# Optimization experiments

Hardware: AMD Instinct MI355X
Metric: run time of the kernel (lower is better)

The kernel has to match this reference:

```python
import jax, jax.numpy as jnp
import numpy as np

I, H, W, S = 1024, 1024, 128, 64


def setup_inputs() -> dict:
    key = jax.random.key(0)
    ks = jax.random.split(key, 20)
    s = 1.0 / np.sqrt(H)  # torch LSTM/Linear init scale
    d = {
        "inputs": jax.random.normal(ks[0], (S, W, I), jnp.float32),
        "h1": jax.random.normal(ks[1], (H,), jnp.float32),
        "c1": jax.random.normal(ks[2], (H,), jnp.float32),
        "h2": jax.random.normal(ks[3], (H,), jnp.float32),
        "c2": jax.random.normal(ks[4], (H,), jnp.float32),
        "Wih1": jax.random.normal(ks[5], (4 * H, I), jnp.float32) * s,
        "Whh1": jax.random.normal(ks[6], (4 * H, H), jnp.float32) * s,
        "bih1": jax.random.normal(ks[7], (4 * H,), jnp.float32) * s,
        "bhh1": jax.random.normal(ks[8], (4 * H,), jnp.float32) * s,
        "Wih2": jax.random.normal(ks[9], (4 * H, H), jnp.float32) * s,
        "Whh2": jax.random.normal(ks[10], (4 * H, H), jnp.float32) * s,
        "bih2": jax.random.normal(ks[11], (4 * H,), jnp.float32) * s,
        "bhh2": jax.random.normal(ks[12], (4 * H,), jnp.float32) * s,
        "att_words": jax.random.normal(ks[13], (W,), jnp.float32),
        "att_sents": jax.random.normal(ks[14], (S,), jnp.float32),
        "Wf": jax.random.normal(ks[15], (1, H), jnp.float32) * s,
        "bf": jax.random.normal(ks[16], (1,), jnp.float32) * s,
    }
    return d


def _lstm_cell(x, h, c, Wih, Whh, bih, bhh):
    # torch gate order: i, f, g, o
    g = x @ Wih.T + h @ Whh.T + bih + bhh  # (4H,)
    i, f, gg, o = jnp.split(g, 4)
    c2 = jax.nn.sigmoid(f) * c + jax.nn.sigmoid(i) * jnp.tanh(gg)
    h2 = jax.nn.sigmoid(o) * jnp.tanh(c2)
    return h2, c2


def reference(inputs, h1, c1, h2, c2, Wih1, Whh1, bih1, bhh1,
              Wih2, Whh2, bih2, bhh2, att_words, att_sents, Wf, bf):
    aw = jax.nn.softmax(att_words)   # (W,)
    asn = jax.nn.softmax(att_sents)  # (S,)

    def word_step(carry, x):
        h, c = carry
        h, c = _lstm_cell(x, h, c, Wih1, Whh1, bih1, bhh1)
        return (h, c), h

    def sent_step(carry, sent):  # sent: (W, I)
        carry, hs = jax.lax.scan(word_step, carry, sent)  # hs: (W, H)
        enc = aw @ hs  # attention pooling over words -> (H,)
        # original detaches hidden state between sentences (forward identity)
        carry = (jax.lax.stop_gradient(carry[0]), jax.lax.stop_gradient(carry[1]))
        return carry, enc

    _, encs = jax.lax.scan(sent_step, (h1, c1), inputs)  # (S, H)

    def sent_lstm_step(carry, x):
        h, c = carry
        h, c = _lstm_cell(x, h, c, Wih2, Whh2, bih2, bhh2)
        return (h, c), h

    _, hs2 = jax.lax.scan(sent_lstm_step, (h2, c2), encs)  # (S, H)
    row = asn @ hs2  # (H,)
    out = jax.nn.sigmoid(row @ Wf.T + bf)  # (1,)
    return out.reshape(1, 1)
```

## Files before the change

### kernel.cpp

```cpp
#include <hip/hip_runtime.h>
#include <hip/hip_bf16.h>

#define NWG 256
#define NTH 256
#define T1  8192
#define SS  64
#define WW  128

typedef unsigned long long u64;
typedef unsigned int u32x4 __attribute__((ext_vector_type(4)));


__device__ __forceinline__ u64 aload(const u64* p) {
  return __hip_atomic_load(p, __ATOMIC_RELAXED, __HIP_MEMORY_SCOPE_AGENT);
}
__device__ __forceinline__ void aswap(u64* p, u64 v) {
  (void)__hip_atomic_exchange(p, v, __ATOMIC_RELAXED, __HIP_MEMORY_SCOPE_AGENT);
}
__device__ __forceinline__ u64 pack(float v, unsigned tag) {
  return ((u64)tag << 32) | (u64)__float_as_uint(v);
}
__device__ __forceinline__ float ftanh(float x) {
  return 1.f - 2.f / (1.f + __expf(2.f * x));
}

__device__ __forceinline__ void load32_sc1(const u64* p, u32x4& a, u32x4& b) {
  asm volatile("global_load_dwordx4 %0, %2, off sc1\n\t"
               "global_load_dwordx4 %1, %2, off offset:16 sc1\n\t"
               "s_waitcnt vmcnt(0)"
               : "=&v"(a), "=&v"(b) : "v"(p) : "memory");
}

#define SPIN4(BASE, TAG, DST) do {                                        \
    const u64* _q = (BASE) + ((size_t)tid << 2);                          \
    const unsigned _t = (unsigned)(TAG); u32x4 _a, _b;                    \
    for (;;) { load32_sc1(_q, _a, _b);                                    \
      if (__builtin_expect(_a.y == _t && _a.w == _t &&                    \
                           _b.y == _t && _b.w == _t, 1)) break; }         \
    float* _d = (DST) + (tid << 2);                                       \
    _d[0] = __uint_as_float(_a.x); _d[1] = __uint_as_float(_a.z);         \
    _d[2] = __uint_as_float(_b.x); _d[3] = __uint_as_float(_b.z);         \
  } while (0)

__global__ __launch_bounds__(NTH) __attribute__((amdgpu_waves_per_eu(1, 1)))
void lstm_hier_attn(const float* __restrict__ xin,
                    const float* __restrict__ h1_0, const float* __restrict__ c1_0,
                    const float* __restrict__ h2_0, const float* __restrict__ c2_0,
                    const float* __restrict__ Wih1, const float* __restrict__ Whh1,
                    const float* __restrict__ bih1, const float* __restrict__ bhh1,
                    const float* __restrict__ Wih2, const float* __restrict__ Whh2,
                    const float* __restrict__ bih2, const float* __restrict__ bhh2,
                    const float* __restrict__ attw, const float* __restrict__ atts,
                    const float* __restrict__ Wf,   const float* __restrict__ bfb,
                    u64* hbuf64, u64* encs64, u64* part64, float* out)
{
  const int wid = blockIdx.x;
  const int tid = threadIdx.x;
  const int wv  = tid >> 6;
  const int l   = tid & 63;
  const int u0  = wid << 2;

  __shared__ float wih_lds[16 * 1024];
  __shared__ float h_lds[2][1024];
  __shared__ float e_lds[2][1024];
  __shared__ float aw_lds[WW];
  __shared__ float as_lds[SS];
  __shared__ float fin_lds[4];

  if (tid == 0) {
    float m = -1e30f;
    for (int i = 0; i < WW; ++i) m = fmaxf(m, attw[i]);
    float ssum = 0.f;
    for (int i = 0; i < WW; ++i) { float e = __expf(attw[i] - m); aw_lds[i] = e; ssum += e; }
    float inv = 1.f / ssum;
    for (int i = 0; i < WW; ++i) aw_lds[i] *= inv;
    m = -1e30f;
    for (int i = 0; i < SS; ++i) m = fmaxf(m, atts[i]);
    ssum = 0.f;
    for (int i = 0; i < SS; ++i) { float e = __expf(atts[i] - m); as_lds[i] = e; ssum += e; }
    inv = 1.f / ssum;
    for (int i = 0; i < SS; ++i) as_lds[i] *= inv;
  }

  for (int q = 0; q < 64; ++q) {
    const int idx = (q << 8) + tid;
    const int rr = idx >> 10, col = idx & 1023;
    wih_lds[idx] = Wih1[(size_t)(((rr >> 2) << 10) + u0 + (rr & 3)) * 1024 + col];
  }
  float whh[4][16], bias[4];
#pragma unroll
  for (int g = 0; g < 4; ++g) {
    const int grow = (g << 10) + u0 + wv;
    bias[g] = bih1[grow] + bhh1[grow];
    const float* ph = Whh1 + (size_t)grow * 1024 + l;
#pragma unroll
    for (int m = 0; m < 16; ++m) whh[g][m] = ph[m << 6];
  }
#pragma unroll
  for (int g = 0; g < 4; ++g)
#pragma unroll
    for (int m = 0; m < 16; ++m) asm volatile("" : "+v"(whh[g][m]));

  float c   = c1_0[u0 + wv];
  float enc = 0.f, row = 0.f;
  const int rb0 = (0 + wv) << 10, rb1 = (4 + wv) << 10,
            rb2 = (8 + wv) << 10, rb3 = (12 + wv) << 10;
  __syncthreads();

  for (int k = 0; k < T1; ++k) {
    const int p = k & 1;
    const float* xrow = xin + (size_t)k * 1024;
    float a0 = 0.f, a1 = 0.f, a2 = 0.f, a3 = 0.f;
#pragma unroll
    for (int m = 0; m < 16; ++m) {
      const int cix = (m << 6) + l;
      const float x = xrow[cix];
      a0 += wih_lds[rb0 + cix] * x; a1 += wih_lds[rb1 + cix] * x;
      a2 += wih_lds[rb2 + cix] * x; a3 += wih_lds[rb3 + cix] * x;
    }

    if (k > 0) { SPIN4(hbuf64 + ((size_t)p << 10), k, h_lds[p]); }
    else {
      const float* s = h1_0 + (tid << 2); float* d = h_lds[0] + (tid << 2);
      d[0] = s[0]; d[1] = s[1]; d[2] = s[2]; d[3] = s[3];
    }
    __syncthreads();

#pragma unroll
    for (int m = 0; m < 16; ++m) {
      const float hv = h_lds[p][(m << 6) + l];
      a0 += whh[0][m] * hv; a1 += whh[1][m] * hv;
      a2 += whh[2][m] * hv; a3 += whh[3][m] * hv;
    }
#pragma unroll
    for (int mm = 1; mm < 64; mm <<= 1) {
      a0 += __shfl_xor(a0, mm); a1 += __shfl_xor(a1, mm);
      a2 += __shfl_xor(a2, mm); a3 += __shfl_xor(a3, mm);
    }
    const float ig = a0 + bias[0], fg = a1 + bias[1];
    const float gg = a2 + bias[2], og = a3 + bias[3];
    const float si = 1.f / (1.f + __expf(-ig));
    const float sf = 1.f / (1.f + __expf(-fg));
    const float so = 1.f / (1.f + __expf(-og));
    c = sf * c + si * ftanh(gg);
    const float h = so * ftanh(c);
    if (l == 0)
      aswap(&hbuf64[((size_t)((k + 1) & 1) << 10) + u0 + wv],
            pack(h, (unsigned)(k + 1)));
    const int wd = k & (WW - 1);
    const float e_new = enc + aw_lds[wd] * h;
    if (wd == WW - 1) {
      if (l == 0)
        aswap(&encs64[((size_t)(k >> 7) << 10) + u0 + wv],
              pack(e_new, (unsigned)((k >> 7) + 1)));
      enc = 0.f;
    } else enc = e_new;
  }

  __syncthreads();
  for (int q = 0; q < 64; ++q) {
    const int idx = (q << 8) + tid;
    const int rr = idx >> 10, col = idx & 1023;
    wih_lds[idx] = Wih2[(size_t)(((rr >> 2) << 10) + u0 + (rr & 3)) * 1024 + col];
  }
#pragma unroll
  for (int g = 0; g < 4; ++g) {
    const int grow = (g << 10) + u0 + wv;
    bias[g] = bih2[grow] + bhh2[grow];
    const float* ph = Whh2 + (size_t)grow * 1024 + l;
#pragma unroll
    for (int m = 0; m < 16; ++m) whh[g][m] = ph[m << 6];
  }
#pragma unroll
  for (int g = 0; g < 4; ++g)
#pragma unroll
    for (int m = 0; m < 16; ++m) asm volatile("" : "+v"(whh[g][m]));
  c = c2_0[u0 + wv];

  for (int s2 = 0; s2 < SS; ++s2) {
    const unsigned kg = (unsigned)(T1 + s2);
    const int p = (int)(kg & 1), pe = s2 & 1;
    SPIN4(encs64 + ((size_t)s2 << 10), (unsigned)(s2 + 1), e_lds[pe]);
    SPIN4(hbuf64 + ((size_t)p << 10), kg, h_lds[p]);
    if (s2 == 0) {
      const float* s = h2_0 + (tid << 2); float* d = h_lds[0] + (tid << 2);
      d[0] = s[0]; d[1] = s[1]; d[2] = s[2]; d[3] = s[3];
    }
    __syncthreads();

    float a0 = 0.f, a1 = 0.f, a2 = 0.f, a3 = 0.f;
#pragma unroll
    for (int m = 0; m < 16; ++m) {
      const int cix = (m << 6) + l;
      const float ev = e_lds[pe][cix];
      a0 += wih_lds[rb0 + cix] * ev; a1 += wih_lds[rb1 + cix] * ev;
      a2 += wih_lds[rb2 + cix] * ev; a3 += wih_lds[rb3 + cix] * ev;
      const float hv = h_lds[p][cix];
      a0 += whh[0][m] * hv; a1 += whh[1][m] * hv;
      a2 += whh[2][m] * hv; a3 += whh[3][m] * hv;
    }
#pragma unroll
    for (int mm = 1; mm < 64; mm <<= 1) {
      a0 += __shfl_xor(a0, mm); a1 += __shfl_xor(a1, mm);
      a2 += __shfl_xor(a2, mm); a3 += __shfl_xor(a3, mm);
    }
    const float ig = a0 + bias[0], fg = a1 + bias[1];
    const float gg = a2 + bias[2], og = a3 + bias[3];
    const float si = 1.f / (1.f + __expf(-ig));
    const float sf = 1.f / (1.f + __expf(-fg));
    const float so = 1.f / (1.f + __expf(-og));
    c = sf * c + si * ftanh(gg);
    const float h = so * ftanh(c);
    if (l == 0)
      aswap(&hbuf64[((size_t)((kg + 1) & 1) << 10) + u0 + wv], pack(h, kg + 1u));
    row += as_lds[s2] * h;
  }

  if (l == 0) fin_lds[wv] = row * Wf[u0 + wv];
  __syncthreads();
  if (tid == 0)
    aswap(&part64[wid],
          pack(fin_lds[0] + fin_lds[1] + fin_lds[2] + fin_lds[3], 1u));
  if (wid == 0) {
    u64 a;
    for (;;) { a = aload(&part64[tid]); if ((unsigned)(a >> 32) == 1u) break; }
    e_lds[0][tid] = __uint_as_float((unsigned)a);
    __syncthreads();
    if (wv == 0) {
      float pp = e_lds[0][l] + e_lds[0][64 + l] + e_lds[0][128 + l] + e_lds[0][192 + l];
#pragma unroll
      for (int mm = 1; mm < 64; mm <<= 1) pp += __shfl_xor(pp, mm);
      if (l == 0) out[0] = 1.f / (1.f + __expf(-(pp + bfb[0])));
    }
  }
}

extern "C" void kernel_launch(void* const* d_in, const int* in_sizes, int n_in,
                              void* d_out, int out_size, void* d_ws, size_t ws_size,
                              hipStream_t stream) {
  (void)in_sizes; (void)n_in; (void)out_size; (void)ws_size;
  const float* xin  = (const float*)d_in[0];
  const float* h1   = (const float*)d_in[1];
  const float* c1   = (const float*)d_in[2];
  const float* h2   = (const float*)d_in[3];
  const float* c2   = (const float*)d_in[4];
  const float* Wih1 = (const float*)d_in[5];
  const float* Whh1 = (const float*)d_in[6];
  const float* bih1 = (const float*)d_in[7];
  const float* bhh1 = (const float*)d_in[8];
  const float* Wih2 = (const float*)d_in[9];
  const float* Whh2 = (const float*)d_in[10];
  const float* bih2 = (const float*)d_in[11];
  const float* bhh2 = (const float*)d_in[12];
  const float* attw = (const float*)d_in[13];
  const float* atts = (const float*)d_in[14];
  const float* Wf   = (const float*)d_in[15];
  const float* bfb  = (const float*)d_in[16];

  u64* hbuf64 = (u64*)d_ws;
  u64* encs64 = hbuf64 + 2048;
  u64* part64 = encs64 + 65536;
  float* out  = (float*)d_out;

  hipMemsetAsync(d_ws, 0, (2048 + 65536 + 256) * sizeof(u64), stream);
  lstm_hier_attn<<<dim3(NWG), dim3(NTH), 0, stream>>>(
      xin, h1, c1, h2, c2, Wih1, Whh1, bih1, bhh1,
      Wih2, Whh2, bih2, bhh2, attw, atts, Wf, bfb,
      hbuf64, encs64, part64, out);
}
```

Baseline: 16.65 ms.

## Halve workgroup count and exchange hidden state as packed fp16 pairs

Regroups the persistent kernel from 256 workgroups of 4 waves into 128 workgroups of 8 waves, so each workgroup owns 8 hidden units and holds twice as many Wih rows in LDS. Each workgroup gathers its 8 new h values in LDS and publishes them as four tagged fp16-pair words. Readers then poll half as many 16-byte slots per step. The goal is to shrink the grid-wide spin-exchange payload and the number of participants in the per-step handoff. The cost is an extra __syncthreads per step, two waves per SIMD competing for compute, and fp16 rounding of the recurrent hidden state.

```diff
diff --git a/kernel.cpp b/kernel.cpp
--- a/kernel.cpp
+++ b/kernel.cpp
@@ -1,8 +1,8 @@
 #include <hip/hip_runtime.h>
-#include <hip/hip_bf16.h>
-
-#define NWG 256
-#define NTH 256
+#include <hip/hip_fp16.h>
+
+#define NWG 128
+#define NTH 512
 #define T1  8192
 #define SS  64
 #define WW  128
@@ -17,32 +17,29 @@
 __device__ __forceinline__ void aswap(u64* p, u64 v) {
   (void)__hip_atomic_exchange(p, v, __ATOMIC_RELAXED, __HIP_MEMORY_SCOPE_AGENT);
 }
-__device__ __forceinline__ u64 pack(float v, unsigned tag) {
+__device__ __forceinline__ u64 packf(float v, unsigned tag) {
   return ((u64)tag << 32) | (u64)__float_as_uint(v);
+}
+__device__ __forceinline__ unsigned pk2(float a, float b) {
+  __half2 h = __floats2half2_rn(a, b);
+  return *(unsigned*)&h;
+}
+__device__ __forceinline__ float2 upk2(unsigned u) {
+  __half2 h = *(__half2*)&u;
+  return __half22float2(h);
 }
 __device__ __forceinline__ float ftanh(float x) {
   return 1.f - 2.f / (1.f + __expf(2.f * x));
 }
 
-__device__ __forceinline__ void load32_sc1(const u64* p, u32x4& a, u32x4& b) {
-  asm volatile("global_load_dwordx4 %0, %2, off sc1\n\t"
-               "global_load_dwordx4 %1, %2, off offset:16 sc1\n\t"
-               "s_waitcnt vmcnt(0)"
-               : "=&v"(a), "=&v"(b) : "v"(p) : "memory");
-}
-
-#define SPIN4(BASE, TAG, DST) do {                                        \
-    const u64* _q = (BASE) + ((size_t)tid << 2);                          \
-    const unsigned _t = (unsigned)(TAG); u32x4 _a, _b;                    \
-    for (;;) { load32_sc1(_q, _a, _b);                                    \
-      if (__builtin_expect(_a.y == _t && _a.w == _t &&                    \
-                           _b.y == _t && _b.w == _t, 1)) break; }         \
-    float* _d = (DST) + (tid << 2);                                       \
-    _d[0] = __uint_as_float(_a.x); _d[1] = __uint_as_float(_a.z);         \
-    _d[2] = __uint_as_float(_b.x); _d[3] = __uint_as_float(_b.z);         \
-  } while (0)
-
-__global__ __launch_bounds__(NTH) __attribute__((amdgpu_waves_per_eu(1, 1)))
+__device__ __forceinline__ u32x4 load16_sc1(const void* p) {
+  u32x4 r;
+  asm volatile("global_load_dwordx4 %0, %1, off sc1\n\ts_waitcnt vmcnt(0)"
+               : "=&v"(r) : "v"(p) : "memory");
+  return r;
+}
+
+__global__ __launch_bounds__(NTH) __attribute__((amdgpu_waves_per_eu(2, 2)))
 void lstm_hier_attn(const float* __restrict__ xin,
                     const float* __restrict__ h1_0, const float* __restrict__ c1_0,
                     const float* __restrict__ h2_0, const float* __restrict__ c2_0,
@@ -58,14 +55,15 @@
   const int tid = threadIdx.x;
   const int wv  = tid >> 6;
   const int l   = tid & 63;
-  const int u0  = wid << 2;
-
-  __shared__ float wih_lds[16 * 1024];
+  const int u0  = wid << 3;
+
+  __shared__ float wih_lds[32 * 1024];
   __shared__ float h_lds[2][1024];
   __shared__ float e_lds[2][1024];
   __shared__ float aw_lds[WW];
   __shared__ float as_lds[SS];
-  __shared__ float fin_lds[4];
+  __shared__ float h_out[8];
+  __shared__ float fin_lds[8];
 
   if (tid == 0) {
     float m = -1e30f;
@@ -83,9 +81,9 @@
   }
 
   for (int q = 0; q < 64; ++q) {
-    const int idx = (q << 8) + tid;
+    const int idx = (q << 9) + tid;
     const int rr = idx >> 10, col = idx & 1023;
-    wih_lds[idx] = Wih1[(size_t)(((rr >> 2) << 10) + u0 + (rr & 3)) * 1024 + col];
+    wih_lds[idx] = Wih1[(size_t)(((rr >> 3) << 10) + u0 + (rr & 7)) * 1024 + col];
   }
   float whh[4][16], bias[4];
 #pragma unroll
@@ -103,8 +101,8 @@
 
   float c   = c1_0[u0 + wv];
   float enc = 0.f, row = 0.f;
-  const int rb0 = (0 + wv) << 10, rb1 = (4 + wv) << 10,
-            rb2 = (8 + wv) << 10, rb3 = (12 + wv) << 10;
+  const int rb0 = (0 * 8 + wv) << 10, rb1 = (1 * 8 + wv) << 10,
+            rb2 = (2 * 8 + wv) << 10, rb3 = (3 * 8 + wv) << 10;
   __syncthreads();
 
   for (int k = 0; k < T1; ++k) {
@@ -119,10 +117,20 @@
       a2 += wih_lds[rb2 + cix] * x; a3 += wih_lds[rb3 + cix] * x;
     }
 
-    if (k > 0) { SPIN4(hbuf64 + ((size_t)p << 10), k, h_lds[p]); }
-    else {
-      const float* s = h1_0 + (tid << 2); float* d = h_lds[0] + (tid << 2);
-      d[0] = s[0]; d[1] = s[1]; d[2] = s[2]; d[3] = s[3];
+    if (k > 0) {
+      if (tid < 256) {
+        const u64* q = hbuf64 + ((size_t)p << 9) + (tid << 1);
+        const unsigned t = (unsigned)k;
+        u32x4 r;
+        for (;;) { r = load16_sc1(q);
+          if (__builtin_expect(r.y == t && r.w == t, 1)) break; }
+        const float2 ha = upk2(r.x), hb = upk2(r.z);
+        float* d = h_lds[p] + (tid << 2);
+        d[0] = ha.x; d[1] = ha.y; d[2] = hb.x; d[3] = hb.y;
+      }
+    } else {
+      h_lds[0][(tid << 1) + 0] = h1_0[(tid << 1) + 0];
+      h_lds[0][(tid << 1) + 1] = h1_0[(tid << 1) + 1];
     }
     __syncthreads();
 
@@ -144,24 +152,27 @@
     const float so = 1.f / (1.f + __expf(-og));
     c = sf * c + si * ftanh(gg);
     const float h = so * ftanh(c);
-    if (l == 0)
-      aswap(&hbuf64[((size_t)((k + 1) & 1) << 10) + u0 + wv],
-            pack(h, (unsigned)(k + 1)));
+    if (l == 0) h_out[wv] = h;
+    __syncthreads();
+    if (tid < 4)
+      aswap(&hbuf64[((size_t)((k + 1) & 1) << 9) + (wid << 2) + tid],
+            ((u64)(unsigned)(k + 1) << 32) |
+            (u64)pk2(h_out[(tid << 1)], h_out[(tid << 1) + 1]));
     const int wd = k & (WW - 1);
     const float e_new = enc + aw_lds[wd] * h;
     if (wd == WW - 1) {
       if (l == 0)
         aswap(&encs64[((size_t)(k >> 7) << 10) + u0 + wv],
-              pack(e_new, (unsigned)((k >> 7) + 1)));
+              packf(e_new, (unsigned)((k >> 7) + 1)));
       enc = 0.f;
     } else enc = e_new;
   }
 
   __syncthreads();
   for (int q = 0; q < 64; ++q) {
-    const int idx = (q << 8) + tid;
+    const int idx = (q << 9) + tid;
     const int rr = idx >> 10, col = idx & 1023;
-    wih_lds[idx] = Wih2[(size_t)(((rr >> 2) << 10) + u0 + (rr & 3)) * 1024 + col];
+    wih_lds[idx] = Wih2[(size_t)(((rr >> 3) << 10) + u0 + (rr & 7)) * 1024 + col];
   }
 #pragma unroll
   for (int g = 0; g < 4; ++g) {
@@ -180,11 +191,27 @@
   for (int s2 = 0; s2 < SS; ++s2) {
     const unsigned kg = (unsigned)(T1 + s2);
     const int p = (int)(kg & 1), pe = s2 & 1;
-    SPIN4(encs64 + ((size_t)s2 << 10), (unsigned)(s2 + 1), e_lds[pe]);
-    SPIN4(hbuf64 + ((size_t)p << 10), kg, h_lds[p]);
+    {
+      const u64* q = encs64 + ((size_t)s2 << 10) + (tid << 1);
+      const unsigned t = (unsigned)(s2 + 1);
+      u32x4 r;
+      for (;;) { r = load16_sc1(q);
+        if (__builtin_expect(r.y == t && r.w == t, 1)) break; }
+      e_lds[pe][(tid << 1) + 0] = __uint_as_float(r.x);
+      e_lds[pe][(tid << 1) + 1] = __uint_as_float(r.z);
+    }
+    if (tid < 256) {
+      const u64* q = hbuf64 + ((size_t)p << 9) + (tid << 1);
+      u32x4 r;
+      for (;;) { r = load16_sc1(q);
+        if (__builtin_expect(r.y == kg && r.w == kg, 1)) break; }
+      const float2 ha = upk2(r.x), hb = upk2(r.z);
+      float* d = h_lds[p] + (tid << 2);
+      d[0] = ha.x; d[1] = ha.y; d[2] = hb.x; d[3] = hb.y;
+    }
     if (s2 == 0) {
-      const float* s = h2_0 + (tid << 2); float* d = h_lds[0] + (tid << 2);
-      d[0] = s[0]; d[1] = s[1]; d[2] = s[2]; d[3] = s[3];
+      h_lds[0][(tid << 1) + 0] = h2_0[(tid << 1) + 0];
+      h_lds[0][(tid << 1) + 1] = h2_0[(tid << 1) + 1];
     }
     __syncthreads();
 
@@ -211,23 +238,32 @@
     const float so = 1.f / (1.f + __expf(-og));
     c = sf * c + si * ftanh(gg);
     const float h = so * ftanh(c);
-    if (l == 0)
-      aswap(&hbuf64[((size_t)((kg + 1) & 1) << 10) + u0 + wv], pack(h, kg + 1u));
+    if (l == 0) h_out[wv] = h;
+    __syncthreads();
+    if (tid < 4)
+      aswap(&hbuf64[((size_t)((kg + 1) & 1) << 9) + (wid << 2) + tid],
+            ((u64)(kg + 1u) << 32) |
+            (u64)pk2(h_out[(tid << 1)], h_out[(tid << 1) + 1]));
     row += as_lds[s2] * h;
   }
 
   if (l == 0) fin_lds[wv] = row * Wf[u0 + wv];
   __syncthreads();
-  if (tid == 0)
-    aswap(&part64[wid],
-          pack(fin_lds[0] + fin_lds[1] + fin_lds[2] + fin_lds[3], 1u));
+  if (tid == 0) {
+    float pp = 0.f;
+#pragma unroll
+    for (int j = 0; j < 8; ++j) pp += fin_lds[j];
+    aswap(&part64[wid], packf(pp, 1u));
+  }
   if (wid == 0) {
-    u64 a;
-    for (;;) { a = aload(&part64[tid]); if ((unsigned)(a >> 32) == 1u) break; }
-    e_lds[0][tid] = __uint_as_float((unsigned)a);
+    if (tid < NWG) {
+      u64 a;
+      for (;;) { a = aload(&part64[tid]); if ((unsigned)(a >> 32) == 1u) break; }
+      e_lds[0][tid] = __uint_as_float((unsigned)a);
+    }
     __syncthreads();
     if (wv == 0) {
-      float pp = e_lds[0][l] + e_lds[0][64 + l] + e_lds[0][128 + l] + e_lds[0][192 + l];
+      float pp = e_lds[0][l] + e_lds[0][64 + l];
 #pragma unroll
       for (int mm = 1; mm < 64; mm <<= 1) pp += __shfl_xor(pp, mm);
       if (l == 0) out[0] = 1.f / (1.f + __expf(-(pp + bfb[0])));
@@ -258,11 +294,11 @@
   const float* bfb  = (const float*)d_in[16];
 
   u64* hbuf64 = (u64*)d_ws;
-  u64* encs64 = hbuf64 + 2048;
+  u64* encs64 = hbuf64 + 1024;
   u64* part64 = encs64 + 65536;
   float* out  = (float*)d_out;
 
-  hipMemsetAsync(d_ws, 0, (2048 + 65536 + 256) * sizeof(u64), stream);
+  hipMemsetAsync(d_ws, 0, (1024 + 65536 + 128) * sizeof(u64), stream);
   lstm_hier_attn<<<dim3(NWG), dim3(NTH), 0, stream>>>(
       xin, h1, c1, h2, c2, Wih1, Whh1, bih1, bhh1,
       Wih2, Whh2, bih2, bhh2, attw, atts, Wf, bfb,
```

After: 15.67 ms, median of 2. 1.06x faster.
